# Kernel optimization log

Hardware: AMD Instinct MI355X
Metric: run time of the kernel (lower is better)

## Reference

```python
import jax, jax.numpy as jnp
import numpy as np

ALPHA = 0.2  # LeakyReLU negative slope
NEG_INF = -9e15


def _xavier(key, shape, gain=1.414):
    fan_in, fan_out = shape[-2], shape[-1]
    lim = gain * np.sqrt(6.0 / (fan_in + fan_out))
    return jax.random.uniform(key, shape, jnp.float32, -lim, lim)


def setup_inputs() -> dict:
    key = jax.random.key(0)
    ks = jax.random.split(key, 8)
    B, N, Din, H, Dh, Do = 8, 1024, 256, 4, 128, 64
    x = jax.random.normal(ks[0], (B, N, Din), jnp.float32)
    adj = jax.random.randint(ks[1], (B, N, N), 0, 2).astype(jnp.int32)
    W_heads = _xavier(ks[2], (H, Din, Dh))                 # per-head W
    a_heads = _xavier(ks[3], (H, 2 * Dh, 1))[..., 0]       # per-head a, [H, 2*Dh]
    W_out = _xavier(ks[4], (H * Dh, Do))                   # out_att W
    a_out = _xavier(ks[5], (2 * Do, 1))[..., 0]            # out_att a, [2*Do]
    Wf = _xavier(ks[6], (Do, Do), gain=1.0)                # fc_out linear
    bf = jnp.zeros((Do,), jnp.float32)
    return {"x": x, "adj": adj, "W_heads": W_heads, "a_heads": a_heads,
            "W_out": W_out, "a_out": a_out, "Wf": Wf, "bf": bf}


def _leaky_relu(v):
    return jnp.where(v >= 0, v, ALPHA * v)


def _gat(h, adj, W, a):
    # h: [B,N,Fin], adj: [B,N,N], W: [Fin,Fout], a: [2*Fout]
    Wh = h @ W                                   # [B,N,F]
    F = W.shape[-1]
    # additive attention: e_ij = leakyrelu(a_src.Wh_i + a_dst.Wh_j)
    src = Wh @ a[:F]                             # [B,N]
    dst = Wh @ a[F:]                             # [B,N]
    e = _leaky_relu(src[:, :, None] + dst[:, None, :])   # [B,N,N]
    scores = jnp.where(adj > 0, e, NEG_INF)
    attn = jax.nn.softmax(scores, axis=-1)       # dropout is a no-op in eval
    return attn @ Wh                             # [B,N,F]


def reference(x, adj, W_heads, a_heads, W_out, a_out, Wf, bf):
    B, N, _ = x.shape
    H, _, Dh = W_heads.shape
    # multi-head GAT, heads vmapped over leading axis of W_heads / a_heads
    heads = jax.vmap(_gat, in_axes=(None, None, 0, 0))(x, adj, W_heads, a_heads)  # [H,B,N,Dh]
    xcat = jnp.moveaxis(heads, 0, 2).reshape(B, N, H * Dh)   # concat heads, dim=2
    out = jax.nn.elu(_gat(xcat, adj, W_out, a_out))           # [B,N,Do]
    out = jax.nn.relu(out @ Wf + bf)                          # fc_out (dropout no-op)
    return out
```

## Files before the change

### kernel.cpp

```cpp
#include <hip/hip_runtime.h>
#include <hip/hip_bf16.h>

#define BSZ 8
#define NN 1024
#define DIN 256
#define NH 4
#define DH 128
#define DOUT 64
#define RTOT (BSZ*NN)
#define FCAT (NH*DH)
#define ALPHA 0.2f
#define XBLK 1024

typedef unsigned short ushortT;
typedef __attribute__((ext_vector_type(8))) short bf16x8;
typedef __attribute__((ext_vector_type(4))) float f32x4;

static __device__ __forceinline__ ushortT f2bf(float f) {
    __hip_bfloat16 h = __float2bfloat16(f);
    return *reinterpret_cast<ushortT*>(&h);
}
static __device__ __forceinline__ float bfu2f(ushortT u) {
    return __uint_as_float(((unsigned)u) << 16);
}
static __device__ __forceinline__ void split2(float v, ushortT& hi, ushortT& lo) {
    hi = f2bf(v);
    lo = f2bf(v - bfu2f(hi));
}
static __device__ __forceinline__ void gload16(const ushortT* g, ushortT* l) {
    __builtin_amdgcn_global_load_lds(
        (const __attribute__((address_space(1))) unsigned int*)(const void*)g,
        (__attribute__((address_space(3))) unsigned int*)(void*)l, 16, 0, 0);
}

__global__ __launch_bounds__(256) void k_prepw(const float* __restrict__ x,
                                               const float* __restrict__ W,
                                               const float* __restrict__ Wout,
                                               ushortT* __restrict__ xbh, ushortT* __restrict__ xbl,
                                               ushortT* __restrict__ WbTh, ushortT* __restrict__ WbTl,
                                               ushortT* __restrict__ WoTh, ushortT* __restrict__ WoTl) {
    const int bx = blockIdx.x;
    if (bx < XBLK) {
        const int g = bx * 256 + threadIdx.x;
        const float4* p = (const float4*)x + (size_t)g * 2;
        union { ushortT u[8]; uint4 q; } th, tl;
#pragma unroll
        for (int e4 = 0; e4 < 2; ++e4) {
            const float4 v = p[e4];
            split2(v.x, th.u[e4 * 4 + 0], tl.u[e4 * 4 + 0]);
            split2(v.y, th.u[e4 * 4 + 1], tl.u[e4 * 4 + 1]);
            split2(v.z, th.u[e4 * 4 + 2], tl.u[e4 * 4 + 2]);
            split2(v.w, th.u[e4 * 4 + 3], tl.u[e4 * 4 + 3]);
        }
        ((uint4*)xbh)[g] = th.q;
        ((uint4*)xbl)[g] = tl.q;
        return;
    }
    const int g2 = (bx - XBLK) * 256 + threadIdx.x;
    if (g2 < NH * DH * DIN) {
        const int h = g2 >> 15, f = (g2 >> 8) & 127, k = g2 & 255;
        const int kt = k >> 6, k64 = k & 63;
        const float v = W[(size_t)h * DIN * DH + (size_t)k * DH + f];
        ushortT hi, lo; split2(v, hi, lo);
        const int idx = ((h * 4 + kt) * 128 + f) * 64 + k64;
        WbTh[idx] = hi; WbTl[idx] = lo;
    } else {
        const int g3 = g2 - NH * DH * DIN;
        const int f = g3 >> 9, k = g3 & 511;
        const float v = Wout[(size_t)k * DOUT + f];
        ushortT hi, lo; split2(v, hi, lo);
        WoTh[g3] = hi; WoTl[g3] = lo;
    }
}

__global__ __launch_bounds__(512) void k_main(const ushortT* __restrict__ xbh,
                                              const ushortT* __restrict__ xbl,
                                              const float* __restrict__ ah_,
                                              const ushortT* __restrict__ WbTh,
                                              const ushortT* __restrict__ WbTl,
                                              const int* __restrict__ adj,
                                              unsigned* __restrict__ adjbit,
                                              ushortT* __restrict__ WhT,
                                              float* __restrict__ src1,
                                              float* __restrict__ dst1) {
    __shared__ ushortT Ah[128 * 64], Al[128 * 64];
    __shared__ ushortT Bh[128 * 64], Bl[128 * 64];
    __shared__ float sred[8][32], dred[8][32];
    const int tid = threadIdx.x;
    if (blockIdx.x >= 256) {
        const int g = (blockIdx.x - 256) * 512 + tid;
        const int row = g >> 5, w = g & 31;
        const int4* p = (const int4*)(adj + (size_t)row * NN + w * 32);
        unsigned m = 0;
#pragma unroll
        for (int q = 0; q < 8; ++q) {
            const int4 v = p[q];
            m |= (v.x > 0 ? 1u : 0u) << (q * 4 + 0);
            m |= (v.y > 0 ? 1u : 0u) << (q * 4 + 1);
            m |= (v.z > 0 ? 1u : 0u) << (q * 4 + 2);
            m |= (v.w > 0 ? 1u : 0u) << (q * 4 + 3);
        }
        adjbit[g] = m;
        return;
    }
    const int lane = tid & 63, wave = tid >> 6;
    const int h = blockIdx.x >> 6, mt = blockIdx.x & 63;
    const int r0 = mt * 128, b = r0 >> 10, jr = r0 & 1023;
    const int m16 = lane & 15, quad = lane >> 4;
    const int mg = wave >> 1, fg = wave & 1;
    f32x4 acc[2][4];
#pragma unroll
    for (int a = 0; a < 2; ++a)
#pragma unroll
        for (int c = 0; c < 4; ++c) acc[a][c] = (f32x4){0.f, 0.f, 0.f, 0.f};

    for (int kt = 0; kt < 4; ++kt) {
        __syncthreads();
        const ushortT* planeH = WbTh + (size_t)((h * 4 + kt) * 128) * 64;
        const ushortT* planeL = WbTl + (size_t)((h * 4 + kt) * 128) * 64;
#pragma unroll
        for (int half = 0; half < 2; ++half) {
            const int f = wave * 16 + half * 8 + (lane >> 3);
            const int sc = (lane & 7) ^ (f & 7);
            gload16(planeH + (size_t)f * 64 + sc * 8, Bh + (wave * 16 + half * 8) * 64);
            gload16(planeL + (size_t)f * 64 + sc * 8, Bl + (wave * 16 + half * 8) * 64);
        }
#pragma unroll
        for (int half = 0; half < 2; ++half) {
            const int r = wave * 16 + half * 8 + (lane >> 3);
            const int sc = (lane & 7) ^ (r & 7);
            gload16(xbh + (size_t)(r0 + r) * DIN + kt * 64 + sc * 8, Ah + (wave * 16 + half * 8) * 64);
            gload16(xbl + (size_t)(r0 + r) * DIN + kt * 64 + sc * 8, Al + (wave * 16 + half * 8) * 64);
        }
        __syncthreads();
#pragma unroll
        for (int ks = 0; ks < 2; ++ks) {
            bf16x8 a_h[2], a_l[2], b_h[4], b_l[4];
#pragma unroll
            for (int ms = 0; ms < 2; ++ms) {
                const int row = (mg * 2 + ms) * 16 + m16;
                const int cl = (ks * 4 + quad) ^ (row & 7);
                a_h[ms] = *(const bf16x8*)&Ah[row * 64 + cl * 8];
                a_l[ms] = *(const bf16x8*)&Al[row * 64 + cl * 8];
            }
#pragma unroll
            for (int fs = 0; fs < 4; ++fs) {
                const int row = (fg * 4 + fs) * 16 + m16;
                const int cl = (ks * 4 + quad) ^ (row & 7);
                b_h[fs] = *(const bf16x8*)&Bh[row * 64 + cl * 8];
                b_l[fs] = *(const bf16x8*)&Bl[row * 64 + cl * 8];
            }
#pragma unroll
            for (int ms = 0; ms < 2; ++ms)
#pragma unroll
                for (int fs = 0; fs < 4; ++fs) {
                    acc[ms][fs] = __builtin_amdgcn_mfma_f32_16x16x32_bf16(a_h[ms], b_h[fs], acc[ms][fs], 0, 0, 0);
                    acc[ms][fs] = __builtin_amdgcn_mfma_f32_16x16x32_bf16(a_h[ms], b_l[fs], acc[ms][fs], 0, 0, 0);
                    acc[ms][fs] = __builtin_amdgcn_mfma_f32_16x16x32_bf16(a_l[ms], b_h[fs], acc[ms][fs], 0, 0, 0);
                }
        }
    }
    float sacc[2][4] = {{0,0,0,0},{0,0,0,0}}, dacc[2][4] = {{0,0,0,0},{0,0,0,0}};
#pragma unroll
    for (int ms = 0; ms < 2; ++ms)
#pragma unroll
        for (int fs = 0; fs < 4; ++fs) {
            const int fl = (fg * 4 + fs) * 16 + m16;
            const float a_s = ah_[h * 2 * DH + fl];
            const float a_d = ah_[h * 2 * DH + DH + fl];
            union { ushortT u[4]; uint2 q; } tw;
#pragma unroll
            for (int reg = 0; reg < 4; ++reg) {
                const float v = acc[ms][fs][reg];
                sacc[ms][reg] += v * a_s;
                dacc[ms][reg] += v * a_d;
                tw.u[reg] = f2bf(v);
            }
            *(uint2*)(WhT + ((size_t)((b * NH + h) * DH + fl)) * NN + jr + (mg * 2 + ms) * 16 + quad * 4) = tw.q;
        }
#pragma unroll
    for (int ms = 0; ms < 2; ++ms) {
#pragma unroll
        for (int reg = 0; reg < 4; ++reg) {
            float s = sacc[ms][reg], d = dacc[ms][reg];
#pragma unroll
            for (int o = 8; o > 0; o >>= 1) {
                s += __shfl_xor(s, o, 64);
                d += __shfl_xor(d, o, 64);
            }
            if (m16 == 0) {
                sred[wave][ms * 16 + quad * 4 + reg] = s;
                dred[wave][ms * 16 + quad * 4 + reg] = d;
            }
        }
    }
    __syncthreads();
    if (tid < 128) {
        const int mgr = tid >> 5, idx = tid & 31;
        src1[h * RTOT + r0 + tid] = sred[mgr * 2][idx] + sred[mgr * 2 + 1][idx];
        dst1[h * RTOT + r0 + tid] = dred[mgr * 2][idx] + dred[mgr * 2 + 1][idx];
    }
}

__global__ __launch_bounds__(512) void k_attn1(const unsigned* __restrict__ adjbit,
                                               const ushortT* __restrict__ WhT,
                                               const float* __restrict__ src1,
                                               const float* __restrict__ dst1,
                                               ushortT* __restrict__ xcat) {
    __shared__ ushortT As[2][64 * 64];
    __shared__ ushortT Bs[2][128 * 64];
    __shared__ unsigned maskS[64 * 32];
    __shared__ float dstv[NN];
    __shared__ float srcv[64], rowinv[64], red8[8];
    const int tid = threadIdx.x, lane = tid & 63, wave = tid >> 6;
    const int bh = blockIdx.x & 31, it = blockIdx.x >> 5;
    const int b = bh >> 2, h = bh & 3;
    const int i0 = it * 64;
    const int m16 = lane & 15, quad = lane >> 4;
    const int mg = wave >> 2, fg = wave & 3;

    const unsigned* mbase = adjbit + (size_t)(b * NN + i0) * 32;
#pragma unroll
    for (int k2 = 0; k2 < 4; ++k2) maskS[tid + 512 * k2] = mbase[tid + 512 * k2];
    float lm = -INFINITY;
#pragma unroll
    for (int k2 = 0; k2 < 2; ++k2) {
        const float d = dst1[h * RTOT + b * NN + tid + 512 * k2];
        dstv[tid + 512 * k2] = d;
        lm = fmaxf(lm, d);
    }
    if (tid < 64) srcv[tid] = src1[h * RTOT + b * NN + i0 + tid];
#pragma unroll
    for (int o = 32; o > 0; o >>= 1) lm = fmaxf(lm, __shfl_xor(lm, o, 64));
    if (lane == 0) red8[wave] = lm;
    __syncthreads();
    float dmax = red8[0];
#pragma unroll
    for (int w = 1; w < 8; ++w) dmax = fmaxf(dmax, red8[w]);

    const int arow = tid >> 3, apart = tid & 7;
    const float si = srcv[arow];
    float mrow = si + dmax;
    mrow = mrow >= 0.f ? mrow : ALPHA * mrow;
    float fsum = 0.f;

    const ushortT* Bbase = WhT + (size_t)(bh * DH) * NN;
    f32x4 acc[2][2];
#pragma unroll
    for (int a = 0; a < 2; ++a)
#pragma unroll
        for (int c = 0; c < 2; ++c) acc[a][c] = (f32x4){0.f, 0.f, 0.f, 0.f};

#define STAGE_TILE(kt_, buf_)                                                              \
    {                                                                                      \
        const int kt__ = (kt_);                                                            \
        ushortT* bdst = &Bs[(buf_)][0];                                                    \
        _Pragma("unroll")                                                                  \
        for (int half = 0; half < 2; ++half) {                                             \
            const int f = wave * 16 + half * 8 + (lane >> 3);                              \
            gload16(Bbase + (size_t)f * NN + kt__ * 64 + (((lane & 7) ^ (f & 7)) * 8),     \
                    bdst + (wave * 16 + half * 8) * 64);                                   \
        }                                                                                  \
        const unsigned w0 = maskS[arow * 32 + kt__ * 2 + (apart >> 2)];                    \
        const int bb = (apart & 3) * 8;                                                    \
        union { ushortT u[8]; uint4 q; } tw;                                               \
        _Pragma("unroll")                                                                  \
        for (int e4 = 0; e4 < 2; ++e4) {                                                   \
            const float4 dv = *(const float4*)&dstv[kt__ * 64 + apart * 8 + e4 * 4];       \
            const float vv[4] = {dv.x, dv.y, dv.z, dv.w};                                  \
            _Pragma("unroll")                                                              \
            for (int e = 0; e < 4; ++e) {                                                  \
                float v = si + vv[e];                                                      \
                v = v >= 0.f ? v : ALPHA * v;                                              \
                const unsigned bit = (w0 >> (bb + e4 * 4 + e)) & 1u;                       \
                const float p = bit ? __expf(v - mrow) : 0.f;                              \
                fsum += p;                                                                 \
                tw.u[e4 * 4 + e] = f2bf(p);                                                \
            }                                                                              \
        }                                                                                  \
        *(uint4*)&As[(buf_)][arow * 64 + (apart ^ (arow & 7)) * 8] = tw.q;                 \
    }

    STAGE_TILE(0, 0);
    for (int kt = 0; kt < 16; ++kt) {
        const int cb = kt & 1;
        __syncthreads();
        if (kt < 15) STAGE_TILE(kt + 1, cb ^ 1);
#pragma unroll
        for (int ks = 0; ks < 2; ++ks) {
            bf16x8 afr[2];
#pragma unroll
            for (int ms = 0; ms < 2; ++ms) {
                const int rowa = mg * 32 + ms * 16 + m16;
                const int cla = (ks * 4 + quad) ^ (rowa & 7);
                afr[ms] = *(const bf16x8*)&As[cb][rowa * 64 + cla * 8];
            }
#pragma unroll
            for (int ff = 0; ff < 2; ++ff) {
                const int rowb = fg * 32 + ff * 16 + m16;
                const int clb = (ks * 4 + quad) ^ (rowb & 7);
                const bf16x8 bfr = *(const bf16x8*)&Bs[cb][rowb * 64 + clb * 8];
#pragma unroll
                for (int ms = 0; ms < 2; ++ms)
                    acc[ms][ff] = __builtin_amdgcn_mfma_f32_16x16x32_bf16(afr[ms], bfr, acc[ms][ff], 0, 0, 0);
            }
        }
    }
#undef STAGE_TILE
#pragma unroll
    for (int o = 1; o < 8; o <<= 1) fsum += __shfl_xor(fsum, o, 64);
    if ((lane & 7) == 0) rowinv[arow] = 1.f / fsum;
    __syncthreads();
#pragma unroll
    for (int ms = 0; ms < 2; ++ms) {
        float rv[4];
#pragma unroll
        for (int reg = 0; reg < 4; ++reg) rv[reg] = rowinv[mg * 32 + ms * 16 + quad * 4 + reg];
#pragma unroll
        for (int ff = 0; ff < 2; ++ff) {
            const int f = h * DH + fg * 32 + ff * 16 + m16;
#pragma unroll
            for (int reg = 0; reg < 4; ++reg) {
                const int i = i0 + mg * 32 + ms * 16 + quad * 4 + reg;
                xcat[(size_t)(b * NN + i) * FCAT + f] = f2bf(acc[ms][ff][reg] * rv[reg]);
            }
        }
    }
}

__global__ __launch_bounds__(256) void k_wh2(const ushortT* __restrict__ xcat,
                                             const ushortT* __restrict__ WoTh,
                                             const ushortT* __restrict__ WoTl,
                                             const float* __restrict__ aout,
                                             ushortT* __restrict__ Wh2T,
                                             float* __restrict__ src2,
                                             float* __restrict__ dst2) {
    __shared__ ushortT As[32 * 64];
    __shared__ ushortT Bh[64 * 64], Bl[64 * 64];
    __shared__ float sred[4][16], dred[4][16];
    const int tid = threadIdx.x, lane = tid & 63, wave = tid >> 6;
    const int r0 = blockIdx.x * 32;
    const int b = r0 >> 10, jr = r0 & 1023;
    const int m16 = lane & 15, quad = lane >> 4;
    const int mg = wave >> 1, fg = wave & 1;
    f32x4 acc[2] = {(f32x4){0.f,0.f,0.f,0.f}, (f32x4){0.f,0.f,0.f,0.f}};

    for (int kt = 0; kt < 8; ++kt) {
        __syncthreads();
        {
            const int row = wave * 8 + (lane >> 3);
            const int sc = (lane & 7) ^ (row & 7);
            gload16(xcat + (size_t)(r0 + row) * FCAT + kt * 64 + sc * 8, As + wave * 8 * 64);
        }
#pragma unroll
        for (int half = 0; half < 2; ++half) {
            const int f = wave * 16 + half * 8 + (lane >> 3);
            const int sc = (lane & 7) ^ (f & 7);
            gload16(WoTh + (size_t)f * FCAT + kt * 64 + sc * 8, Bh + (wave * 16 + half * 8) * 64);
            gload16(WoTl + (size_t)f * FCAT + kt * 64 + sc * 8, Bl + (wave * 16 + half * 8) * 64);
        }
        __syncthreads();
#pragma unroll
        for (int ks = 0; ks < 2; ++ks) {
            const int rowa = mg * 16 + m16;
            const int cla = (ks * 4 + quad) ^ (rowa & 7);
            const bf16x8 afr = *(const bf16x8*)&As[rowa * 64 + cla * 8];
#pragma unroll
            for (int ff = 0; ff < 2; ++ff) {
                const int rowb = fg * 32 + ff * 16 + m16;
                const int clb = (ks * 4 + quad) ^ (rowb & 7);
                const bf16x8 b_h = *(const bf16x8*)&Bh[rowb * 64 + clb * 8];
                const bf16x8 b_l = *(const bf16x8*)&Bl[rowb * 64 + clb * 8];
                acc[ff] = __builtin_amdgcn_mfma_f32_16x16x32_bf16(afr, b_h, acc[ff], 0, 0, 0);
                acc[ff] = __builtin_amdgcn_mfma_f32_16x16x32_bf16(afr, b_l, acc[ff], 0, 0, 0);
            }
        }
    }
    float sv[4] = {0, 0, 0, 0}, dv[4] = {0, 0, 0, 0};
#pragma unroll
    for (int ff = 0; ff < 2; ++ff) {
        const int f = fg * 32 + ff * 16 + m16;
        const float a_s = aout[f], a_d = aout[DOUT + f];
        union { ushortT u[4]; uint2 q; } tw;
#pragma unroll
        for (int reg = 0; reg < 4; ++reg) {
            const float v = acc[ff][reg];
            sv[reg] += v * a_s;
            dv[reg] += v * a_d;
            tw.u[reg] = f2bf(v);
        }
        *(uint2*)(Wh2T + ((size_t)(b * DOUT + f)) * NN + jr + mg * 16 + quad * 4) = tw.q;
    }
#pragma unroll
    for (int reg = 0; reg < 4; ++reg) {
#pragma unroll
        for (int o = 8; o > 0; o >>= 1) {
            sv[reg] += __shfl_xor(sv[reg], o, 64);
            dv[reg] += __shfl_xor(dv[reg], o, 64);
        }
        if (m16 == 0) { sred[wave][quad * 4 + reg] = sv[reg]; dred[wave][quad * 4 + reg] = dv[reg]; }
    }
    __syncthreads();
    if (tid < 32) {
        const int mgr = tid >> 4, idx = tid & 15;
        src2[r0 + tid] = sred[mgr * 2][idx] + sred[mgr * 2 + 1][idx];
        dst2[r0 + tid] = dred[mgr * 2][idx] + dred[mgr * 2 + 1][idx];
    }
}

__global__ __launch_bounds__(256) void k_attn2(const unsigned* __restrict__ adjbit,
                                               const ushortT* __restrict__ Wh2T,
                                               const float* __restrict__ src2,
                                               const float* __restrict__ dst2,
                                               const float* __restrict__ Wf,
                                               const float* __restrict__ bfv,
                                               float* __restrict__ out) {
    __shared__ ushortT As[2][32 * 64];
    __shared__ ushortT Bs[2][64 * 64];
    __shared__ unsigned maskS[32 * 32];
    __shared__ float dstv[NN];
    __shared__ ushortT Wfh[64 * 64], Wfl[64 * 64];
    __shared__ float t2s[32 * 68];
    __shared__ float srcv[32], rowinv[32], red4[4];
    const int tid = threadIdx.x, lane = tid & 63, wave = tid >> 6;
    const int b = blockIdx.x & 7, it = blockIdx.x >> 3;
    const int i0 = it * 32;
    const int m16 = lane & 15, quad = lane >> 4;

    const unsigned* mbase = adjbit + (size_t)(b * NN + i0) * 32;
#pragma unroll
    for (int k2 = 0; k2 < 4; ++k2) maskS[tid + 256 * k2] = mbase[tid + 256 * k2];
    float lm = -INFINITY;
#pragma unroll
    for (int k2 = 0; k2 < 4; ++k2) {
        const float d = dst2[b * NN + tid + 256 * k2];
        dstv[tid + 256 * k2] = d;
        lm = fmaxf(lm, d);
    }
    if (tid < 32) srcv[tid] = src2[b * NN + i0 + tid];
    {
        const int c = tid & 63, kc = (tid >> 6) * 16;
        union { ushortT u[16]; uint4 q[2]; } th, tl;
#pragma unroll
        for (int e = 0; e < 16; ++e)
            split2(Wf[(size_t)(kc + e) * DOUT + c], th.u[e], tl.u[e]);
        const int s0 = ((tid >> 6) * 2) ^ (c & 7), s1 = ((tid >> 6) * 2 + 1) ^ (c & 7);
        *(uint4*)&Wfh[c * 64 + s0 * 8] = th.q[0];
        *(uint4*)&Wfh[c * 64 + s1 * 8] = th.q[1];
        *(uint4*)&Wfl[c * 64 + s0 * 8] = tl.q[0];
        *(uint4*)&Wfl[c * 64 + s1 * 8] = tl.q[1];
    }
#pragma unroll
    for (int o = 32; o > 0; o >>= 1) lm = fmaxf(lm, __shfl_xor(lm, o, 64));
    if (lane == 0) red4[wave] = lm;
    __syncthreads();
    const float dmax = fmaxf(fmaxf(red4[0], red4[1]), fmaxf(red4[2], red4[3]));

    const int arow = tid >> 3, apart = tid & 7;
    const float si = srcv[arow];
    float mrow = si + dmax;
    mrow = mrow >= 0.f ? mrow : ALPHA * mrow;
    float fsum = 0.f;

    const int mfrag = wave >> 1, fh = wave & 1;
    const ushortT* Bbase = Wh2T + (size_t)(b * DOUT) * NN;
    f32x4 acc[2] = {(f32x4){0.f,0.f,0.f,0.f}, (f32x4){0.f,0.f,0.f,0.f}};

#define STAGE2(kt_, buf_)                                                                  \
    {                                                                                      \
        const int kt__ = (kt_);                                                            \
        ushortT* bdst = &Bs[(buf_)][0];                                                    \
        _Pragma("unroll")                                                                  \
        for (int half = 0; half < 2; ++half) {                                             \
            const int f = wave * 16 + half * 8 + (lane >> 3);                              \
            gload16(Bbase + (size_t)f * NN + kt__ * 64 + (((lane & 7) ^ (f & 7)) * 8),     \
                    bdst + (wave * 16 + half * 8) * 64);                                   \
        }                                                                                  \
        const unsigned w0 = maskS[arow * 32 + kt__ * 2 + (apart >> 2)];                    \
        const int bb = (apart & 3) * 8;                                                    \
        union { ushortT u[8]; uint4 q; } tw;                                               \
        _Pragma("unroll")                                                                  \
        for (int e4 = 0; e4 < 2; ++e4) {                                                   \
            const float4 dv = *(const float4*)&dstv[kt__ * 64 + apart * 8 + e4 * 4];       \
            const float vv[4] = {dv.x, dv.y, dv.z, dv.w};                                  \
            _Pragma("unroll")                                                              \
            for (int e = 0; e < 4; ++e) {                                                  \
                float v = si + vv[e];                                                      \
                v = v >= 0.f ? v : ALPHA * v;                                              \
                const unsigned bit = (w0 >> (bb + e4 * 4 + e)) & 1u;                       \
                const float p = bit ? __expf(v - mrow) : 0.f;                              \
                fsum += p;                                                                 \
                tw.u[e4 * 4 + e] = f2bf(p);                                                \
            }                                                                              \
        }                                                                                  \
        *(uint4*)&As[(buf_)][arow * 64 + (apart ^ (arow & 7)) * 8] = tw.q;                 \
    }

    STAGE2(0, 0);
    for (int kt = 0; kt < 16; ++kt) {
        const int cb = kt & 1;
        __syncthreads();
        if (kt < 15) STAGE2(kt + 1, cb ^ 1);
#pragma unroll
        for (int ks = 0; ks < 2; ++ks) {
            const int rowa = mfrag * 16 + m16;
            const int cla = (ks * 4 + quad) ^ (rowa & 7);
            const bf16x8 afr = *(const bf16x8*)&As[cb][rowa * 64 + cla * 8];
#pragma unroll
            for (int ff = 0; ff < 2; ++ff) {
                const int rowb = (fh * 2 + ff) * 16 + m16;
                const int clb = (ks * 4 + quad) ^ (rowb & 7);
                const bf16x8 bfr = *(const bf16x8*)&Bs[cb][rowb * 64 + clb * 8];
                acc[ff] = __builtin_amdgcn_mfma_f32_16x16x32_bf16(afr, bfr, acc[ff], 0, 0, 0);
            }
        }
    }
#undef STAGE2
#pragma unroll
    for (int o = 1; o < 8; o <<= 1) fsum += __shfl_xor(fsum, o, 64);
    if ((lane & 7) == 0) rowinv[arow] = 1.f / fsum;
    __syncthreads();
#pragma unroll
    for (int ff = 0; ff < 2; ++ff) {
#pragma unroll
        for (int reg = 0; reg < 4; ++reg) {
            const int row = mfrag * 16 + quad * 4 + reg;
            float v = acc[ff][reg] * rowinv[row];
            v = v > 0.f ? v : (__expf(v) - 1.f);
            t2s[row * 68 + (fh * 2 + ff) * 16 + m16] = v;
        }
    }
    __syncthreads();
    const int mf = wave >> 1, nh = wave & 1;
    f32x4 oacc[2];
#pragma unroll
    for (int g = 0; g < 2; ++g) {
        const float bias = bfv[(nh * 2 + g) * 16 + m16];
        oacc[g] = (f32x4){bias, bias, bias, bias};
    }
#pragma unroll
    for (int ks = 0; ks < 2; ++ks) {
        const int rowa = mf * 16 + m16;
        const float4 fA = *(const float4*)&t2s[rowa * 68 + ks * 32 + quad * 8];
        const float4 fB = *(const float4*)&t2s[rowa * 68 + ks * 32 + quad * 8 + 4];
        union { ushortT u[8]; bf16x8 v; } a_h, a_l;
        const float av[8] = {fA.x, fA.y, fA.z, fA.w, fB.x, fB.y, fB.z, fB.w};
#pragma unroll
        for (int e = 0; e < 8; ++e) split2(av[e], a_h.u[e], a_l.u[e]);
#pragma unroll
        for (int g = 0; g < 2; ++g) {
            const int rowc = (nh * 2 + g) * 16 + m16;
            const int cl = (ks * 4 + quad) ^ (rowc & 7);
            const bf16x8 b_h = *(const bf16x8*)&Wfh[rowc * 64 + cl * 8];
            const bf16x8 b_l = *(const bf16x8*)&Wfl[rowc * 64 + cl * 8];
            oacc[g] = __builtin_amdgcn_mfma_f32_16x16x32_bf16(a_h.v, b_h, oacc[g], 0, 0, 0);
            oacc[g] = __builtin_amdgcn_mfma_f32_16x16x32_bf16(a_h.v, b_l, oacc[g], 0, 0, 0);
            oacc[g] = __builtin_amdgcn_mfma_f32_16x16x32_bf16(a_l.v, b_h, oacc[g], 0, 0, 0);
        }
    }
#pragma unroll
    for (int g = 0; g < 2; ++g) {
        const int c = (nh * 2 + g) * 16 + m16;
#pragma unroll
        for (int reg = 0; reg < 4; ++reg) {
            const int i = i0 + mf * 16 + quad * 4 + reg;
            out[(size_t)(b * NN + i) * DOUT + c] = fmaxf(oacc[g][reg], 0.f);
        }
    }
}

extern "C" void kernel_launch(void* const* d_in, const int* in_sizes, int n_in,
                              void* d_out, int out_size, void* d_ws, size_t ws_size,
                              hipStream_t stream) {
    const float* x   = (const float*)d_in[0];
    const int*   adj = (const int*)d_in[1];
    const float* Wh  = (const float*)d_in[2];
    const float* ah  = (const float*)d_in[3];
    const float* Wo  = (const float*)d_in[4];
    const float* ao  = (const float*)d_in[5];
    const float* Wf  = (const float*)d_in[6];
    const float* bf  = (const float*)d_in[7];
    float* out = (float*)d_out;

    float* ws    = (float*)d_ws;
    float* src1  = ws;
    float* dst1  = src1 + NH * RTOT;
    float* src2  = dst1 + NH * RTOT;
    float* dst2  = src2 + RTOT;
    ushortT* WhT   = (ushortT*)(dst2 + RTOT);
    ushortT* Wh2T  = WhT + (size_t)RTOT * FCAT;
    ushortT* xcat  = Wh2T + (size_t)RTOT * DOUT;
    ushortT* WbTh  = xcat + (size_t)RTOT * FCAT;
    ushortT* WbTl  = WbTh + NH * DH * DIN;
    ushortT* WoTh  = WbTl + NH * DH * DIN;
    ushortT* WoTl  = WoTh + DOUT * FCAT;
    unsigned* adjbit = (unsigned*)(WoTl + DOUT * FCAT);
    ushortT* xbh  = (ushortT*)(adjbit + (size_t)BSZ * NN * 32);
    ushortT* xbl  = xbh + (size_t)RTOT * DIN;

    hipLaunchKernelGGL(k_prepw, dim3(XBLK + (NH * DH * DIN + DOUT * FCAT) / 256), dim3(256), 0, stream,
                       x, Wh, Wo, xbh, xbl, WbTh, WbTl, WoTh, WoTl);
    hipLaunchKernelGGL(k_main,  dim3(768), dim3(512), 0, stream,
                       xbh, xbl, ah, WbTh, WbTl, adj, adjbit, WhT, src1, dst1);
    hipLaunchKernelGGL(k_attn1, dim3(512), dim3(512), 0, stream,
                       adjbit, WhT, src1, dst1, xcat);
    hipLaunchKernelGGL(k_wh2,   dim3(256), dim3(256), 0, stream,
                       xcat, WoTh, WoTl, ao, Wh2T, src2, dst2);
    hipLaunchKernelGGL(k_attn2, dim3(256), dim3(256), 0, stream,
                       adjbit, Wh2T, src2, dst2, Wf, bf, out);
}
```

Baseline: 154.1 us.

## Load attention B operands straight to registers and widen attn2 to 512 threads

In both attention kernels the Wh tile is no longer staged through shared memory with async global-to-LDS copies. Each wave now loads its B fragments directly from global into registers, one k-tile ahead, using an unrolled two-buffer loop. k_attn2 also moves from 256 to 512 threads per block, so each wave computes one 16x16 output fragment and softmax staging is split across 16 threads per row. This cuts LDS traffic and footprint, but makes the MFMA inputs depend on uncoalesced, strided global loads whose latency is only partly hidden by the one-tile prefetch.

```diff
diff --git a/kernel.cpp b/kernel.cpp
--- a/kernel.cpp
+++ b/kernel.cpp
@@ -208,7 +208,6 @@
                                                const float* __restrict__ dst1,
                                                ushortT* __restrict__ xcat) {
     __shared__ ushortT As[2][64 * 64];
-    __shared__ ushortT Bs[2][128 * 64];
     __shared__ unsigned maskS[64 * 32];
     __shared__ float dstv[NN];
     __shared__ float srcv[64], rowinv[64], red8[8];
@@ -251,16 +250,9 @@
 #pragma unroll
         for (int c = 0; c < 2; ++c) acc[a][c] = (f32x4){0.f, 0.f, 0.f, 0.f};
 
-#define STAGE_TILE(kt_, buf_)                                                              \
+#define STAGE_A(kt_, buf_)                                                                 \
     {                                                                                      \
         const int kt__ = (kt_);                                                            \
-        ushortT* bdst = &Bs[(buf_)][0];                                                    \
-        _Pragma("unroll")                                                                  \
-        for (int half = 0; half < 2; ++half) {                                             \
-            const int f = wave * 16 + half * 8 + (lane >> 3);                              \
-            gload16(Bbase + (size_t)f * NN + kt__ * 64 + (((lane & 7) ^ (f & 7)) * 8),     \
-                    bdst + (wave * 16 + half * 8) * 64);                                   \
-        }                                                                                  \
         const unsigned w0 = maskS[arow * 32 + kt__ * 2 + (apart >> 2)];                    \
         const int bb = (apart & 3) * 8;                                                    \
         union { ushortT u[8]; uint4 q; } tw;                                               \
@@ -280,33 +272,48 @@
         }                                                                                  \
         *(uint4*)&As[(buf_)][arow * 64 + (apart ^ (arow & 7)) * 8] = tw.q;                 \
     }
-
-    STAGE_TILE(0, 0);
-    for (int kt = 0; kt < 16; ++kt) {
-        const int cb = kt & 1;
-        __syncthreads();
-        if (kt < 15) STAGE_TILE(kt + 1, cb ^ 1);
-#pragma unroll
-        for (int ks = 0; ks < 2; ++ks) {
-            bf16x8 afr[2];
-#pragma unroll
-            for (int ms = 0; ms < 2; ++ms) {
-                const int rowa = mg * 32 + ms * 16 + m16;
-                const int cla = (ks * 4 + quad) ^ (rowa & 7);
-                afr[ms] = *(const bf16x8*)&As[cb][rowa * 64 + cla * 8];
-            }
-#pragma unroll
-            for (int ff = 0; ff < 2; ++ff) {
-                const int rowb = fg * 32 + ff * 16 + m16;
-                const int clb = (ks * 4 + quad) ^ (rowb & 7);
-                const bf16x8 bfr = *(const bf16x8*)&Bs[cb][rowb * 64 + clb * 8];
-#pragma unroll
-                for (int ms = 0; ms < 2; ++ms)
-                    acc[ms][ff] = __builtin_amdgcn_mfma_f32_16x16x32_bf16(afr[ms], bfr, acc[ms][ff], 0, 0, 0);
-            }
-        }
-    }
-#undef STAGE_TILE
+#define LOADB(kt_, dst_)                                                                   \
+    {                                                                                      \
+        _Pragma("unroll")                                                                  \
+        for (int ks = 0; ks < 2; ++ks)                                                     \
+            _Pragma("unroll")                                                              \
+            for (int ff = 0; ff < 2; ++ff)                                                 \
+                dst_[ks][ff] = *(const bf16x8*)(Bbase +                                    \
+                    (size_t)(fg * 32 + ff * 16 + m16) * NN + (kt_) * 64 + (ks * 4 + quad) * 8); \
+    }
+#define MFMA_STEP(buf_, bv_)                                                               \
+    {                                                                                      \
+        _Pragma("unroll")                                                                  \
+        for (int ks = 0; ks < 2; ++ks) {                                                   \
+            bf16x8 afr[2];                                                                 \
+            _Pragma("unroll")                                                              \
+            for (int ms = 0; ms < 2; ++ms) {                                               \
+                const int rowa = mg * 32 + ms * 16 + m16;                                  \
+                const int cla = (ks * 4 + quad) ^ (rowa & 7);                              \
+                afr[ms] = *(const bf16x8*)&As[(buf_)][rowa * 64 + cla * 8];                \
+            }                                                                              \
+            _Pragma("unroll")                                                              \
+            for (int ff = 0; ff < 2; ++ff)                                                 \
+                _Pragma("unroll")                                                          \
+                for (int ms = 0; ms < 2; ++ms)                                             \
+                    acc[ms][ff] = __builtin_amdgcn_mfma_f32_16x16x32_bf16(afr[ms], bv_[ks][ff], acc[ms][ff], 0, 0, 0); \
+        }                                                                                  \
+    }
+
+    bf16x8 b0v[2][2], b1v[2][2];
+    LOADB(0, b0v);
+    STAGE_A(0, 0);
+    for (int kt = 0; kt < 16; kt += 2) {
+        __syncthreads();
+        if (kt < 15) { LOADB(kt + 1, b1v); STAGE_A(kt + 1, 1); }
+        MFMA_STEP(0, b0v);
+        __syncthreads();
+        if (kt < 14) { LOADB(kt + 2, b0v); STAGE_A(kt + 2, 0); }
+        MFMA_STEP(1, b1v);
+    }
+#undef STAGE_A
+#undef LOADB
+#undef MFMA_STEP
 #pragma unroll
     for (int o = 1; o < 8; o <<= 1) fsum += __shfl_xor(fsum, o, 64);
     if ((lane & 7) == 0) rowinv[arow] = 1.f / fsum;
@@ -408,7 +415,7 @@
     }
 }
 
-__global__ __launch_bounds__(256) void k_attn2(const unsigned* __restrict__ adjbit,
+__global__ __launch_bounds__(512) void k_attn2(const unsigned* __restrict__ adjbit,
                                                const ushortT* __restrict__ Wh2T,
                                                const float* __restrict__ src2,
                                                const float* __restrict__ dst2,
@@ -416,12 +423,11 @@
                                                const float* __restrict__ bfv,
                                                float* __restrict__ out) {
     __shared__ ushortT As[2][32 * 64];
-    __shared__ ushortT Bs[2][64 * 64];
+    __shared__ ushortT Wfh[64 * 64], Wfl[64 * 64];
     __shared__ unsigned maskS[32 * 32];
     __shared__ float dstv[NN];
-    __shared__ ushortT Wfh[64 * 64], Wfl[64 * 64];
     __shared__ float t2s[32 * 68];
-    __shared__ float srcv[32], rowinv[32], red4[4];
+    __shared__ float srcv[32], rowinv[32], red8[8];
     const int tid = threadIdx.x, lane = tid & 63, wave = tid >> 6;
     const int b = blockIdx.x & 7, it = blockIdx.x >> 3;
     const int i0 = it * 32;
@@ -429,143 +435,132 @@
 
     const unsigned* mbase = adjbit + (size_t)(b * NN + i0) * 32;
 #pragma unroll
-    for (int k2 = 0; k2 < 4; ++k2) maskS[tid + 256 * k2] = mbase[tid + 256 * k2];
+    for (int k2 = 0; k2 < 2; ++k2) maskS[tid + 512 * k2] = mbase[tid + 512 * k2];
     float lm = -INFINITY;
 #pragma unroll
-    for (int k2 = 0; k2 < 4; ++k2) {
-        const float d = dst2[b * NN + tid + 256 * k2];
-        dstv[tid + 256 * k2] = d;
+    for (int k2 = 0; k2 < 2; ++k2) {
+        const float d = dst2[b * NN + tid + 512 * k2];
+        dstv[tid + 512 * k2] = d;
         lm = fmaxf(lm, d);
     }
     if (tid < 32) srcv[tid] = src2[b * NN + i0 + tid];
     {
-        const int c = tid & 63, kc = (tid >> 6) * 16;
-        union { ushortT u[16]; uint4 q[2]; } th, tl;
-#pragma unroll
-        for (int e = 0; e < 16; ++e)
-            split2(Wf[(size_t)(kc + e) * DOUT + c], th.u[e], tl.u[e]);
-        const int s0 = ((tid >> 6) * 2) ^ (c & 7), s1 = ((tid >> 6) * 2 + 1) ^ (c & 7);
-        *(uint4*)&Wfh[c * 64 + s0 * 8] = th.q[0];
-        *(uint4*)&Wfh[c * 64 + s1 * 8] = th.q[1];
-        *(uint4*)&Wfl[c * 64 + s0 * 8] = tl.q[0];
-        *(uint4*)&Wfl[c * 64 + s1 * 8] = tl.q[1];
+        const int c = tid & 63, kc = wave * 8;
+        union { ushortT u[8]; uint4 q; } th4, tl4;
+#pragma unroll
+        for (int e = 0; e < 8; ++e)
+            split2(Wf[(size_t)(kc + e) * DOUT + c], th4.u[e], tl4.u[e]);
+        const int ch = wave ^ (c & 7);
+        *(uint4*)&Wfh[c * 64 + ch * 8] = th4.q;
+        *(uint4*)&Wfl[c * 64 + ch * 8] = tl4.q;
     }
 #pragma unroll
     for (int o = 32; o > 0; o >>= 1) lm = fmaxf(lm, __shfl_xor(lm, o, 64));
-    if (lane == 0) red4[wave] = lm;
+    if (lane == 0) red8[wave] = lm;
     __syncthreads();
-    const float dmax = fmaxf(fmaxf(red4[0], red4[1]), fmaxf(red4[2], red4[3]));
-
-    const int arow = tid >> 3, apart = tid & 7;
+    float dmax = red8[0];
+#pragma unroll
+    for (int w = 1; w < 8; ++w) dmax = fmaxf(dmax, red8[w]);
+
+    const int arow = tid >> 4, apart = tid & 15;
     const float si = srcv[arow];
     float mrow = si + dmax;
     mrow = mrow >= 0.f ? mrow : ALPHA * mrow;
     float fsum = 0.f;
 
-    const int mfrag = wave >> 1, fh = wave & 1;
+    const int mfrag = wave >> 2, fq = wave & 3;
     const ushortT* Bbase = Wh2T + (size_t)(b * DOUT) * NN;
-    f32x4 acc[2] = {(f32x4){0.f,0.f,0.f,0.f}, (f32x4){0.f,0.f,0.f,0.f}};
-
-#define STAGE2(kt_, buf_)                                                                  \
+    f32x4 acc4 = (f32x4){0.f, 0.f, 0.f, 0.f};
+
+#define STAGE_A2(kt_, buf_)                                                                \
     {                                                                                      \
         const int kt__ = (kt_);                                                            \
-        ushortT* bdst = &Bs[(buf_)][0];                                                    \
+        const unsigned w0 = maskS[arow * 32 + kt__ * 2 + (apart >> 3)];                    \
+        const int bb = (apart & 7) * 4;                                                    \
+        union { ushortT u[4]; uint2 q; } tw;                                               \
+        const float4 dv = *(const float4*)&dstv[kt__ * 64 + apart * 4];                    \
+        const float vv[4] = {dv.x, dv.y, dv.z, dv.w};                                      \
         _Pragma("unroll")                                                                  \
-        for (int half = 0; half < 2; ++half) {                                             \
-            const int f = wave * 16 + half * 8 + (lane >> 3);                              \
-            gload16(Bbase + (size_t)f * NN + kt__ * 64 + (((lane & 7) ^ (f & 7)) * 8),     \
-                    bdst + (wave * 16 + half * 8) * 64);                                   \
+        for (int e = 0; e < 4; ++e) {                                                      \
+            float v = si + vv[e];                                                          \
+            v = v >= 0.f ? v : ALPHA * v;                                                  \
+            const unsigned bit = (w0 >> (bb + e)) & 1u;                                    \
+            const float p = bit ? __expf(v - mrow) : 0.f;                                  \
+            fsum += p;                                                                     \
+            tw.u[e] = f2bf(p);                                                             \
         }                                                                                  \
-        const unsigned w0 = maskS[arow * 32 + kt__ * 2 + (apart >> 2)];                    \
-        const int bb = (apart & 3) * 8;                                                    \
-        union { ushortT u[8]; uint4 q; } tw;                                               \
+        *(uint2*)&As[(buf_)][arow * 64 + (((apart >> 1) ^ (arow & 7)) * 8) + (apart & 1) * 4] = tw.q; \
+    }
+#define LOADB2(kt_, dst_)                                                                  \
+    {                                                                                      \
         _Pragma("unroll")                                                                  \
-        for (int e4 = 0; e4 < 2; ++e4) {                                                   \
-            const float4 dv = *(const float4*)&dstv[kt__ * 64 + apart * 8 + e4 * 4];       \
-            const float vv[4] = {dv.x, dv.y, dv.z, dv.w};                                  \
-            _Pragma("unroll")                                                              \
-            for (int e = 0; e < 4; ++e) {                                                  \
-                float v = si + vv[e];                                                      \
-                v = v >= 0.f ? v : ALPHA * v;                                              \
-                const unsigned bit = (w0 >> (bb + e4 * 4 + e)) & 1u;                       \
-                const float p = bit ? __expf(v - mrow) : 0.f;                              \
-                fsum += p;                                                                 \
-                tw.u[e4 * 4 + e] = f2bf(p);                                                \
-            }                                                                              \
+        for (int ks = 0; ks < 2; ++ks)                                                     \
+            dst_[ks] = *(const bf16x8*)(Bbase +                                            \
+                (size_t)(fq * 16 + m16) * NN + (kt_) * 64 + (ks * 4 + quad) * 8);          \
+    }
+#define MFMA_STEP2(buf_, bv_)                                                              \
+    {                                                                                      \
+        _Pragma("unroll")                                                                  \
+        for (int ks = 0; ks < 2; ++ks) {                                                   \
+            const int rowa = mfrag * 16 + m16;                                             \
+            const int cla = (ks * 4 + quad) ^ (rowa & 7);                                  \
+            const bf16x8 afr = *(const bf16x8*)&As[(buf_)][rowa * 64 + cla * 8];           \
+            acc4 = __builtin_amdgcn_mfma_f32_16x16x32_bf16(afr, bv_[ks], acc4, 0, 0, 0);   \
         }                                                                                  \
-        *(uint4*)&As[(buf_)][arow * 64 + (apart ^ (arow & 7)) * 8] = tw.q;                 \
-    }
-
-    STAGE2(0, 0);
-    for (int kt = 0; kt < 16; ++kt) {
-        const int cb = kt & 1;
-        __syncthreads();
-        if (kt < 15) STAGE2(kt + 1, cb ^ 1);
-#pragma unroll
-        for (int ks = 0; ks < 2; ++ks) {
-            const int rowa = mfrag * 16 + m16;
-            const int cla = (ks * 4 + quad) ^ (rowa & 7);
-            const bf16x8 afr = *(const bf16x8*)&As[cb][rowa * 64 + cla * 8];
-#pragma unroll
-            for (int ff = 0; ff < 2; ++ff) {
-                const int rowb = (fh * 2 + ff) * 16 + m16;
-                const int clb = (ks * 4 + quad) ^ (rowb & 7);
-                const bf16x8 bfr = *(const bf16x8*)&Bs[cb][rowb * 64 + clb * 8];
-                acc[ff] = __builtin_amdgcn_mfma_f32_16x16x32_bf16(afr, bfr, acc[ff], 0, 0, 0);
-            }
-        }
-    }
-#undef STAGE2
-#pragma unroll
-    for (int o = 1; o < 8; o <<= 1) fsum += __shfl_xor(fsum, o, 64);
-    if ((lane & 7) == 0) rowinv[arow] = 1.f / fsum;
+    }
+
+    bf16x8 b0v[2], b1v[2];
+    LOADB2(0, b0v);
+    STAGE_A2(0, 0);
+    for (int kt = 0; kt < 16; kt += 2) {
+        __syncthreads();
+        if (kt < 15) { LOADB2(kt + 1, b1v); STAGE_A2(kt + 1, 1); }
+        MFMA_STEP2(0, b0v);
+        __syncthreads();
+        if (kt < 14) { LOADB2(kt + 2, b0v); STAGE_A2(kt + 2, 0); }
+        MFMA_STEP2(1, b1v);
+    }
+#undef STAGE_A2
+#undef LOADB2
+#undef MFMA_STEP2
+#pragma unroll
+    for (int o = 1; o < 16; o <<= 1) fsum += __shfl_xor(fsum, o, 64);
+    if ((lane & 15) == 0) rowinv[arow] = 1.f / fsum;
     __syncthreads();
 #pragma unroll
-    for (int ff = 0; ff < 2; ++ff) {
-#pragma unroll
-        for (int reg = 0; reg < 4; ++reg) {
-            const int row = mfrag * 16 + quad * 4 + reg;
-            float v = acc[ff][reg] * rowinv[row];
-            v = v > 0.f ? v : (__expf(v) - 1.f);
-            t2s[row * 68 + (fh * 2 + ff) * 16 + m16] = v;
-        }
+    for (int reg = 0; reg < 4; ++reg) {
+        const int row = mfrag * 16 + quad * 4 + reg;
+        float v = acc4[reg] * rowinv[row];
+        v = v > 0.f ? v : (__expf(v) - 1.f);
+        t2s[row * 68 + fq * 16 + m16] = v;
     }
     __syncthreads();
-    const int mf = wave >> 1, nh = wave & 1;
-    f32x4 oacc[2];
-#pragma unroll
-    for (int g = 0; g < 2; ++g) {
-        const float bias = bfv[(nh * 2 + g) * 16 + m16];
-        oacc[g] = (f32x4){bias, bias, bias, bias};
+    const int cc = fq * 16 + m16;
+    f32x4 oacc;
+    {
+        const float bias = bfv[cc];
+        oacc = (f32x4){bias, bias, bias, bias};
     }
 #pragma unroll
     for (int ks = 0; ks < 2; ++ks) {
-        const int rowa = mf * 16 + m16;
+        const int rowa = mfrag * 16 + m16;
         const float4 fA = *(const float4*)&t2s[rowa * 68 + ks * 32 + quad * 8];
         const float4 fB = *(const float4*)&t2s[rowa * 68 + ks * 32 + quad * 8 + 4];
         union { ushortT u[8]; bf16x8 v; } a_h, a_l;
         const float av[8] = {fA.x, fA.y, fA.z, fA.w, fB.x, fB.y, fB.z, fB.w};
 #pragma unroll
         for (int e = 0; e < 8; ++e) split2(av[e], a_h.u[e], a_l.u[e]);
-#pragma unroll
-        for (int g = 0; g < 2; ++g) {
-            const int rowc = (nh * 2 + g) * 16 + m16;
-            const int cl = (ks * 4 + quad) ^ (rowc & 7);
-            const bf16x8 b_h = *(const bf16x8*)&Wfh[rowc * 64 + cl * 8];
-            const bf16x8 b_l = *(const bf16x8*)&Wfl[rowc * 64 + cl * 8];
-            oacc[g] = __builtin_amdgcn_mfma_f32_16x16x32_bf16(a_h.v, b_h, oacc[g], 0, 0, 0);
-            oacc[g] = __builtin_amdgcn_mfma_f32_16x16x32_bf16(a_h.v, b_l, oacc[g], 0, 0, 0);
-            oacc[g] = __builtin_amdgcn_mfma_f32_16x16x32_bf16(a_l.v, b_h, oacc[g], 0, 0, 0);
-        }
-    }
-#pragma unroll
-    for (int g = 0; g < 2; ++g) {
-        const int c = (nh * 2 + g) * 16 + m16;
-#pragma unroll
-        for (int reg = 0; reg < 4; ++reg) {
-            const int i = i0 + mf * 16 + quad * 4 + reg;
-            out[(size_t)(b * NN + i) * DOUT + c] = fmaxf(oacc[g][reg], 0.f);
-        }
+        const int cl = (ks * 4 + quad) ^ (cc & 7);
+        const bf16x8 b_h = *(const bf16x8*)&Wfh[cc * 64 + cl * 8];
+        const bf16x8 b_l = *(const bf16x8*)&Wfl[cc * 64 + cl * 8];
+        oacc = __builtin_amdgcn_mfma_f32_16x16x32_bf16(a_h.v, b_h, oacc, 0, 0, 0);
+        oacc = __builtin_amdgcn_mfma_f32_16x16x32_bf16(a_h.v, b_l, oacc, 0, 0, 0);
+        oacc = __builtin_amdgcn_mfma_f32_16x16x32_bf16(a_l.v, b_h, oacc, 0, 0, 0);
+    }
+#pragma unroll
+    for (int reg = 0; reg < 4; ++reg) {
+        const int i = i0 + mfrag * 16 + quad * 4 + reg;
+        out[(size_t)(b * NN + i) * DOUT + cc] = fmaxf(oacc[reg], 0.f);
     }
 }
 
@@ -606,6 +601,6 @@
                        adjbit, WhT, src1, dst1, xcat);
     hipLaunchKernelGGL(k_wh2,   dim3(256), dim3(256), 0, stream,
                        xcat, WoTh, WoTl, ao, Wh2T, src2, dst2);
-    hipLaunchKernelGGL(k_attn2, dim3(256), dim3(256), 0, stream,
+    hipLaunchKernelGGL(k_attn2, dim3(256), dim3(512), 0, stream,
                        adjbit, Wh2T, src2, dst2, Wf, bf, out);
 }
```

Result: no change. 156.6 us (+1.6%).
